# Optimization experiments

Measured on AMD Instinct MI355X. Metric: run time of the kernel, lower is better.

## Reference

```python
import jax, jax.numpy as jnp
import numpy as np

NUM_EXPERTS = 8
EMBED_DIM = 1024
EXPERT_DIM = 2048
TOP_K = 2
B, T = 2, 1024


def setup_inputs() -> dict:
    key = jax.random.key(0)
    ks = jax.random.split(key, 7)
    std = 0.02
    return {
        "x": jax.random.normal(ks[0], (B, T, EMBED_DIM), dtype=jnp.float32),
        "gate_inputs": jax.random.normal(ks[1], (B, T, EMBED_DIM), dtype=jnp.float32),
        "gate_kernel": jax.random.normal(ks[2], (EMBED_DIM, NUM_EXPERTS), dtype=jnp.float32) * std,
        "per_expert_scale": jnp.ones((NUM_EXPERTS,), dtype=jnp.float32),
        "gate_proj_w": jax.random.normal(ks[3], (NUM_EXPERTS, EMBED_DIM, EXPERT_DIM), dtype=jnp.float32) * std,
        "up_proj_w": jax.random.normal(ks[4], (NUM_EXPERTS, EMBED_DIM, EXPERT_DIM), dtype=jnp.float32) * std,
        "down_proj_w": jax.random.normal(ks[5], (NUM_EXPERTS, EXPERT_DIM, EMBED_DIM), dtype=jnp.float32) * std,
    }


def reference(x, gate_inputs, gate_kernel, per_expert_scale,
              gate_proj_w, up_proj_w, down_proj_w):
    Bb, Tt, D = x.shape
    x_flat = x.reshape(Bb * Tt, D)          # [t, e]
    g_flat = gate_inputs.reshape(Bb * Tt, D)

    logits = jnp.dot(g_flat, gate_kernel)   # [t, n]
    topk_logits, topk_idx = jax.lax.top_k(logits, TOP_K)  # [t, k]
    weights = jax.nn.sigmoid(topk_logits)   # [t, k]

    # Dense all-expert projections (as in the original module)
    gate_out = jnp.einsum('te,ned->tnd', x_flat, gate_proj_w)  # [t, n, d]
    up_out = jnp.einsum('te,ned->tnd', x_flat, up_proj_w)
    act = jax.nn.gelu(gate_out) * up_out
    expert_out = jnp.einsum('tnd,nde->tne', act, down_proj_w)  # [t, n, e]
    expert_out = expert_out * per_expert_scale[None, :, None]

    mask = jax.nn.one_hot(topk_idx, NUM_EXPERTS, dtype=expert_out.dtype)  # [t, k, n]
    selected = jnp.einsum('tkn,tne->tke', mask, expert_out)               # [t, k, e]
    out = jnp.einsum('tk,tke->te', weights, selected)                     # [t, e]
    return out.reshape(Bb, Tt, D)
```

## Files before the change

### kernel.cpp

```cpp
#include <hip/hip_runtime.h>
#include <math.h>
#include <stdint.h>

#define NE 8
#define ED 1024
#define FD 2048
#define NTOK 2048
#define BM 128
#define BN 128
#define BK 64

typedef unsigned short u16;
typedef unsigned int u32;
typedef __attribute__((ext_vector_type(4))) float f32x4;
typedef __attribute__((ext_vector_type(8))) short s16x8;
typedef __attribute__((ext_vector_type(4))) unsigned int u32v4;


__device__ __forceinline__ u16 f2bf(float f) {
    u32 u = __builtin_bit_cast(u32, f);
    u32 r = u + 0x7fffu + ((u >> 16) & 1u);
    return (u16)(r >> 16);
}

typedef __attribute__((address_space(1))) const void gvoid_t;
typedef __attribute__((address_space(3))) void lvoid_t;

__device__ __forceinline__ void gload16(const void* g, void* l) {
    __builtin_amdgcn_global_load_lds((gvoid_t*)g, (lvoid_t*)l, 16, 0, 0);
}


#define WS_CNT 0u
#define WS_OFF 64u
#define WS_TOK 256u
#define WS_WT  65792u
#define WS_XB  131328u
#define WS_WG  (8u << 20)
#define WS_WU  41943040u
#define WS_WD  75497472u
#define WS_ACT 109051904u
#define WS_NEED 130023424u


__global__ __launch_bounds__(256) void k_router(
        const float* __restrict__ gin, const float* __restrict__ gk,
        int* __restrict__ cnt, int* __restrict__ tok, float* __restrict__ wl) {
    int lane = threadIdx.x & 63;
    int t = (blockIdx.x * 256 + threadIdx.x) >> 6;
    if (t >= NTOK) return;
    const float* row = gin + (size_t)t * ED;
    float acc[NE];
#pragma unroll
    for (int e = 0; e < NE; e++) acc[e] = 0.f;
    for (int i = lane; i < ED; i += 64) {
        float v = row[i];
        const float* g = gk + i * NE;
#pragma unroll
        for (int e = 0; e < NE; e++) acc[e] = fmaf(v, g[e], acc[e]);
    }
#pragma unroll
    for (int e = 0; e < NE; e++) {
#pragma unroll
        for (int off = 32; off > 0; off >>= 1)
            acc[e] += __shfl_down(acc[e], off, 64);
    }
    if (lane == 0) {
        int b0 = 0; float v0 = acc[0];
#pragma unroll
        for (int e = 1; e < NE; e++) if (acc[e] > v0) { v0 = acc[e]; b0 = e; }
        int b1 = -1; float v1 = -3.4e38f;
#pragma unroll
        for (int e = 0; e < NE; e++) if (e != b0 && acc[e] > v1) { v1 = acc[e]; b1 = e; }
        float w0 = 1.f / (1.f + __expf(-v0));
        float w1 = 1.f / (1.f + __expf(-v1));
        int p0 = atomicAdd(&cnt[b0], 1);
        tok[b0 * NTOK + p0] = t; wl[b0 * NTOK + p0] = w0;
        int p1 = atomicAdd(&cnt[b1], 1);
        tok[b1 * NTOK + p1] = t; wl[b1 * NTOK + p1] = w1;
    }
}

__global__ void k_scan(const int* __restrict__ cnt, int* __restrict__ off) {
    if (threadIdx.x == 0 && blockIdx.x == 0) {
        int a = 0;
#pragma unroll
        for (int e = 0; e < NE; e++) { off[e] = a; a += (cnt[e] + 127) & ~127; }
        off[NE] = a;
    }
}


__global__ __launch_bounds__(256) void k_cvtx(const float4* __restrict__ x, uint2* __restrict__ xb) {
    int i = blockIdx.x * 256 + threadIdx.x;
    float4 v = x[i];
    uint2 o;
    o.x = (u32)f2bf(v.x) | ((u32)f2bf(v.y) << 16);
    o.y = (u32)f2bf(v.z) | ((u32)f2bf(v.w) << 16);
    xb[i] = o;
}


__global__ __launch_bounds__(256) void k_cvtw(
        const float* __restrict__ wgf, const float* __restrict__ wuf, const float* __restrict__ wdf,
        u16* __restrict__ og, u16* __restrict__ ou, u16* __restrict__ od) {
    int b = blockIdx.x;
    const float* src; u16* dst; int NT, KC, ROW;
    if (b < 2048)      { src = wgf; dst = og; NT = 16; KC = 16; ROW = FD; }
    else if (b < 4096) { b -= 2048; src = wuf; dst = ou; NT = 16; KC = 16; ROW = FD; }
    else               { b -= 4096; src = wdf; dst = od; NT = 8;  KC = 32; ROW = ED; }
    int ib = b;
    int kc = b % KC; int r = b / KC; int nt = r % NT; int e = r / NT;
    const float* base = src + (size_t)e * (size_t)(KC * 64) * ROW + (size_t)kc * 64 * ROW + nt * 128;
    u16* ob = dst + (size_t)ib * 8192;

    int tid = threadIdx.x;
    int p = tid & 7;
    int nsub = (tid >> 3) & 7;
    int w = tid >> 6;
    int k0 = (p ^ nsub) * 8;
    const float* rp = base + (size_t)k0 * ROW;

#pragma unroll
    for (int jg = 0; jg < 4; jg++) {
        int n = jg * 32 + w * 8 + nsub;
        float v[8];
#pragma unroll
        for (int i = 0; i < 8; i++) v[i] = rp[(size_t)i * ROW + n];
        u32 wd[4];
#pragma unroll
        for (int j = 0; j < 4; j++)
            wd[j] = (u32)f2bf(v[2 * j]) | ((u32)f2bf(v[2 * j + 1]) << 16);
        *(u32v4*)(ob + (size_t)n * 64 + p * 8) = (u32v4){wd[0], wd[1], wd[2], wd[3]};
    }
}


__global__ __launch_bounds__(256, 2) void k_passA(
        const u16* __restrict__ xb, const u16* __restrict__ wg, const u16* __restrict__ wu,
        const int* __restrict__ cnt, const int* __restrict__ off,
        const int* __restrict__ tok, u16* __restrict__ act) {
    int e = blockIdx.z, mt = blockIdx.y, nt = blockIdx.x;
    int c = cnt[e];
    if (mt * BM >= c) return;
    int rmax = c - mt * BM; if (rmax > BM) rmax = BM;

    __shared__ u16 sA[BM * BK];
    __shared__ u16 sBg[BN * BK];
    __shared__ u16 sBu[BN * BK];

    int tid = threadIdx.x;
    int lane = tid & 63, wv = tid >> 6;
    int wm = wv >> 1, wn = wv & 1;
    int col = lane & 15, quad = lane >> 4;
    int swz = col & 7;

    f32x4 zero = {0.f, 0.f, 0.f, 0.f};
    f32x4 ag[4][4], au[4][4];
#pragma unroll
    for (int i = 0; i < 4; i++)
#pragma unroll
        for (int j = 0; j < 4; j++) { ag[i][j] = zero; au[i][j] = zero; }

    int am = tid >> 1, ah = tid & 1;
    int ridx = mt * BM + am; if (ridx > c - 1) ridx = c - 1;
    int trow = tok[e * NTOK + ridx];
    const u16* asrc = xb + (size_t)trow * ED + ah * 32;
    u16* adst = sA + am * BK;

    const u16* gg = wg + ((size_t)(e * 16 + nt) * 16) * 8192;
    const u16* gu = wu + ((size_t)(e * 16 + nt) * 16) * 8192;
    const u16* bsrc0 = (wv < 2 ? gg : gu);
    int bhalf = (wv & 1) * 4096;
    u16* bdst = (wv < 2 ? sBg : sBu) + bhalf;

    for (int kc = 0; kc < 16; kc++) {
        __syncthreads();
        const u16* bs = bsrc0 + (size_t)kc * 8192 + bhalf + lane * 8;
#pragma unroll
        for (int i = 0; i < 8; i++)
            gload16(bs + i * 512, bdst + i * 512);
        const u16* as = asrc + kc * 64;
#pragma unroll
        for (int j = 0; j < 4; j++) {
            int pg = (ah * 4 + j) ^ (am & 7);
            *(u32v4*)(adst + pg * 8) = *(const u32v4*)(as + j * 8);
        }
        __syncthreads();
#pragma unroll
        for (int st = 0; st < 2; st++) {
            int poff = ((st * 4 + quad) ^ swz) * 8;
            s16x8 af[4];
#pragma unroll
            for (int mf = 0; mf < 4; mf++)
                af[mf] = *(const s16x8*)(sA + (wm * 64 + mf * 16 + col) * BK + poff);
#pragma unroll
            for (int nf = 0; nf < 4; nf++) {
                int brow = (wn * 64 + nf * 16 + col) * BK + poff;
                s16x8 bg = *(const s16x8*)(sBg + brow);
                s16x8 bu = *(const s16x8*)(sBu + brow);
#pragma unroll
                for (int mf = 0; mf < 4; mf++) {
                    ag[mf][nf] = __builtin_amdgcn_mfma_f32_16x16x32_bf16(af[mf], bg, ag[mf][nf], 0, 0, 0);
                    au[mf][nf] = __builtin_amdgcn_mfma_f32_16x16x32_bf16(af[mf], bu, au[mf][nf], 0, 0, 0);
                }
            }
        }
    }

    int tile = (off[e] >> 7) + mt;
    u16* ab = act + (size_t)tile * (32 * 8192);
#pragma unroll
    for (int mf = 0; mf < 4; mf++) {
#pragma unroll
        for (int reg = 0; reg < 4; reg++) {
            int m = wm * 64 + mf * 16 + quad * 4 + reg;
            if (m < rmax) {
#pragma unroll
                for (int nf = 0; nf < 4; nf++) {
                    float gv = ag[mf][nf][reg];
                    float uv = au[mf][nf][reg];
                    float z = 0.7978845608028654f * (gv + 0.044715f * gv * gv * gv);
                    float ez = __expf(-2.f * fabsf(z));
                    float th = (1.f - ez) / (1.f + ez);
                    th = (z < 0.f) ? -th : th;
                    float a = 0.5f * gv * (1.f + th) * uv;
                    int ng = nt * 128 + wn * 64 + nf * 16 + col;
                    int pos = ((((ng >> 3) & 7) ^ (m & 7)) * 8) | (ng & 7);
                    ab[(size_t)(ng >> 6) * 8192 + (size_t)m * 64 + pos] = f2bf(a);
                }
            }
        }
    }
}


__global__ __launch_bounds__(256, 3) void k_passB(
        const u16* __restrict__ act, const u16* __restrict__ wd,
        const int* __restrict__ cnt, const int* __restrict__ off,
        const int* __restrict__ tok, const float* __restrict__ wl,
        const float* __restrict__ scale, float* __restrict__ out) {
    int e = blockIdx.z, mt = blockIdx.y, nt = blockIdx.x;
    int c = cnt[e];
    if (mt * BM >= c) return;
    int rmax = c - mt * BM; if (rmax > BM) rmax = BM;

    __shared__ u16 sA[BM * BK];
    __shared__ u16 sB[BN * BK];

    int tid = threadIdx.x;
    int lane = tid & 63, wv = tid >> 6;
    int wm = wv >> 1, wn = wv & 1;
    int col = lane & 15, quad = lane >> 4;
    int swz = col & 7;

    f32x4 zero = {0.f, 0.f, 0.f, 0.f};
    f32x4 acc[4][4];
#pragma unroll
    for (int i = 0; i < 4; i++)
#pragma unroll
        for (int j = 0; j < 4; j++) acc[i][j] = zero;

    int tile = (off[e] >> 7) + mt;
    const u16* ga = act + (size_t)tile * (32 * 8192);
    const u16* gb = wd + ((size_t)(e * 8 + nt) * 32) * 8192;
    const u16* src0 = (wv < 2 ? ga : gb);
    int shalf = (wv & 1) * 4096;
    u16* dst0 = (wv < 2 ? sA : sB) + shalf;

    for (int kc = 0; kc < 32; kc++) {
        __syncthreads();
        const u16* s = src0 + (size_t)kc * 8192 + shalf + lane * 8;
#pragma unroll
        for (int i = 0; i < 8; i++)
            gload16(s + i * 512, dst0 + i * 512);
        __syncthreads();
#pragma unroll
        for (int st = 0; st < 2; st++) {
            int poff = ((st * 4 + quad) ^ swz) * 8;
            s16x8 af[4];
#pragma unroll
            for (int mf = 0; mf < 4; mf++)
                af[mf] = *(const s16x8*)(sA + (wm * 64 + mf * 16 + col) * BK + poff);
#pragma unroll
            for (int nf = 0; nf < 4; nf++) {
                int brow = (wn * 64 + nf * 16 + col) * BK + poff;
                s16x8 bf = *(const s16x8*)(sB + brow);
#pragma unroll
                for (int mf = 0; mf < 4; mf++)
                    acc[mf][nf] = __builtin_amdgcn_mfma_f32_16x16x32_bf16(af[mf], bf, acc[mf][nf], 0, 0, 0);
            }
        }
    }

    float sc = scale[e];
    int lbase = e * NTOK + mt * BM;
#pragma unroll
    for (int mf = 0; mf < 4; mf++) {
#pragma unroll
        for (int reg = 0; reg < 4; reg++) {
            int m = wm * 64 + mf * 16 + quad * 4 + reg;
            if (m < rmax) {
                int t = tok[lbase + m];
                float w = wl[lbase + m] * sc;
                float* orow = out + (size_t)t * ED + nt * 128 + wn * 64 + col;
#pragma unroll
                for (int nf = 0; nf < 4; nf++)
                    atomicAdd(orow + nf * 16, acc[mf][nf][reg] * w);
            }
        }
    }
}


extern "C" void kernel_launch(void* const* d_in, const int* in_sizes, int n_in,
                              void* d_out, int out_size, void* d_ws, size_t ws_size,
                              hipStream_t stream) {
    const float* x   = (const float*)d_in[0];
    const float* gin = (const float*)d_in[1];
    const float* gk  = (const float*)d_in[2];
    const float* sc  = (const float*)d_in[3];
    const float* wgf = (const float*)d_in[4];
    const float* wuf = (const float*)d_in[5];
    const float* wdf = (const float*)d_in[6];
    float* out = (float*)d_out;

    if (ws_size < (size_t)WS_NEED) {
        hipMemsetAsync(d_out, 0, (size_t)out_size * sizeof(float), stream);
        return;
    }

    char* ws = (char*)d_ws;
    int*   cnt = (int*)(ws + WS_CNT);
    int*   off = (int*)(ws + WS_OFF);
    int*   tok = (int*)(ws + WS_TOK);
    float* wl  = (float*)(ws + WS_WT);
    u16*   xb  = (u16*)(ws + WS_XB);
    u16*   og  = (u16*)(ws + WS_WG);
    u16*   ou  = (u16*)(ws + WS_WU);
    u16*   od  = (u16*)(ws + WS_WD);
    u16*   act = (u16*)(ws + WS_ACT);

    hipMemsetAsync(cnt, 0, 64, stream);
    hipMemsetAsync(d_out, 0, (size_t)out_size * sizeof(float), stream);

    k_cvtw<<<dim3(6144), dim3(256), 0, stream>>>(wgf, wuf, wdf, og, ou, od);
    k_router<<<dim3(512), dim3(256), 0, stream>>>(gin, gk, cnt, tok, wl);
    k_scan<<<dim3(1), dim3(64), 0, stream>>>(cnt, off);
    k_cvtx<<<dim3(2048), dim3(256), 0, stream>>>((const float4*)x, (uint2*)xb);
    k_passA<<<dim3(16, 16, NE), dim3(256), 0, stream>>>(xb, og, ou, cnt, off, tok, act);
    k_passB<<<dim3(8, 16, NE), dim3(256), 0, stream>>>(act, od, cnt, off, tok, wl, sc, out);
}
```

Baseline: 421.9 us.

## Shrink MoE GEMM N-tiles, split-K down proj, LDS-transpose weight conversion

```diff
diff --git a/kernel.cpp b/kernel.cpp
--- a/kernel.cpp
+++ b/kernel.cpp
@@ -7,7 +7,6 @@
 #define FD 2048
 #define NTOK 2048
 #define BM 128
-#define BN 128
 #define BK 64
 
 typedef unsigned short u16;
@@ -114,19 +113,32 @@
     const float* base = src + (size_t)e * (size_t)(KC * 64) * ROW + (size_t)kc * 64 * ROW + nt * 128;
     u16* ob = dst + (size_t)ib * 8192;
 
+    __shared__ float sl[64 * 128];
     int tid = threadIdx.x;
-    int p = tid & 7;
-    int nsub = (tid >> 3) & 7;
-    int w = tid >> 6;
-    int k0 = (p ^ nsub) * 8;
-    const float* rp = base + (size_t)k0 * ROW;
+
+    {
+        int rb = tid >> 5;
+        int c  = tid & 31;
+        const float* rp = base + (size_t)(8 * rb) * ROW + c * 4;
+        float* lp = sl + (8 * rb) * 128 + ((c ^ rb) << 2);
+#pragma unroll
+        for (int j = 0; j < 8; j++) {
+            float4 v = *(const float4*)(rp + (size_t)j * ROW);
+            *(float4*)(lp + j * 128) = v;
+        }
+    }
+    __syncthreads();
 
 #pragma unroll
     for (int jg = 0; jg < 4; jg++) {
-        int n = jg * 32 + w * 8 + nsub;
+        int o = jg * 256 + tid;
+        int n = o >> 3, p = o & 7;
+        int g = p ^ (n & 7);
+        int w = ((((n >> 2) ^ g) << 2) | (n & 3));
+        const float* kp = sl + (8 * g) * 128 + w;
         float v[8];
 #pragma unroll
-        for (int i = 0; i < 8; i++) v[i] = rp[(size_t)i * ROW + n];
+        for (int j = 0; j < 8; j++) v[j] = kp[j * 128];
         u32 wd[4];
 #pragma unroll
         for (int j = 0; j < 4; j++)
@@ -136,18 +148,19 @@
 }
 
 
-__global__ __launch_bounds__(256, 2) void k_passA(
+__global__ __launch_bounds__(256, 3) void k_passA(
         const u16* __restrict__ xb, const u16* __restrict__ wg, const u16* __restrict__ wu,
         const int* __restrict__ cnt, const int* __restrict__ off,
         const int* __restrict__ tok, u16* __restrict__ act) {
-    int e = blockIdx.z, mt = blockIdx.y, nt = blockIdx.x;
+    int flat = blockIdx.x;
+    int mt = flat >> 8; int rr = flat & 255; int e = rr >> 5; int nt = rr & 31;
     int c = cnt[e];
     if (mt * BM >= c) return;
     int rmax = c - mt * BM; if (rmax > BM) rmax = BM;
 
     __shared__ u16 sA[BM * BK];
-    __shared__ u16 sBg[BN * BK];
-    __shared__ u16 sBu[BN * BK];
+    __shared__ u16 sBg[64 * BK];
+    __shared__ u16 sBu[64 * BK];
 
     int tid = threadIdx.x;
     int lane = tid & 63, wv = tid >> 6;
@@ -156,11 +169,11 @@
     int swz = col & 7;
 
     f32x4 zero = {0.f, 0.f, 0.f, 0.f};
-    f32x4 ag[4][4], au[4][4];
+    f32x4 ag[4][2], au[4][2];
 #pragma unroll
     for (int i = 0; i < 4; i++)
 #pragma unroll
-        for (int j = 0; j < 4; j++) { ag[i][j] = zero; au[i][j] = zero; }
+        for (int j = 0; j < 2; j++) { ag[i][j] = zero; au[i][j] = zero; }
 
     int am = tid >> 1, ah = tid & 1;
     int ridx = mt * BM + am; if (ridx > c - 1) ridx = c - 1;
@@ -168,17 +181,17 @@
     const u16* asrc = xb + (size_t)trow * ED + ah * 32;
     u16* adst = sA + am * BK;
 
-    const u16* gg = wg + ((size_t)(e * 16 + nt) * 16) * 8192;
-    const u16* gu = wu + ((size_t)(e * 16 + nt) * 16) * 8192;
+    const u16* gg = wg + ((size_t)(e * 16 + (nt >> 1)) * 16) * 8192 + (nt & 1) * 4096;
+    const u16* gu = wu + ((size_t)(e * 16 + (nt >> 1)) * 16) * 8192 + (nt & 1) * 4096;
     const u16* bsrc0 = (wv < 2 ? gg : gu);
-    int bhalf = (wv & 1) * 4096;
+    int bhalf = (wv & 1) * 2048;
     u16* bdst = (wv < 2 ? sBg : sBu) + bhalf;
 
     for (int kc = 0; kc < 16; kc++) {
         __syncthreads();
         const u16* bs = bsrc0 + (size_t)kc * 8192 + bhalf + lane * 8;
 #pragma unroll
-        for (int i = 0; i < 8; i++)
+        for (int i = 0; i < 4; i++)
             gload16(bs + i * 512, bdst + i * 512);
         const u16* as = asrc + kc * 64;
 #pragma unroll
@@ -195,8 +208,8 @@
             for (int mf = 0; mf < 4; mf++)
                 af[mf] = *(const s16x8*)(sA + (wm * 64 + mf * 16 + col) * BK + poff);
 #pragma unroll
-            for (int nf = 0; nf < 4; nf++) {
-                int brow = (wn * 64 + nf * 16 + col) * BK + poff;
+            for (int nf = 0; nf < 2; nf++) {
+                int brow = (wn * 32 + nf * 16 + col) * BK + poff;
                 s16x8 bg = *(const s16x8*)(sBg + brow);
                 s16x8 bu = *(const s16x8*)(sBu + brow);
 #pragma unroll
@@ -217,7 +230,7 @@
             int m = wm * 64 + mf * 16 + quad * 4 + reg;
             if (m < rmax) {
 #pragma unroll
-                for (int nf = 0; nf < 4; nf++) {
+                for (int nf = 0; nf < 2; nf++) {
                     float gv = ag[mf][nf][reg];
                     float uv = au[mf][nf][reg];
                     float z = 0.7978845608028654f * (gv + 0.044715f * gv * gv * gv);
@@ -225,9 +238,9 @@
                     float th = (1.f - ez) / (1.f + ez);
                     th = (z < 0.f) ? -th : th;
                     float a = 0.5f * gv * (1.f + th) * uv;
-                    int ng = nt * 128 + wn * 64 + nf * 16 + col;
+                    int ng = nt * 64 + wn * 32 + nf * 16 + col;
                     int pos = ((((ng >> 3) & 7) ^ (m & 7)) * 8) | (ng & 7);
-                    ab[(size_t)(ng >> 6) * 8192 + (size_t)m * 64 + pos] = f2bf(a);
+                    ab[(size_t)nt * 8192 + (size_t)m * 64 + pos] = f2bf(a);
                 }
             }
         }
@@ -235,18 +248,20 @@
 }
 
 
-__global__ __launch_bounds__(256, 3) void k_passB(
+__global__ __launch_bounds__(256, 4) void k_passB(
         const u16* __restrict__ act, const u16* __restrict__ wd,
         const int* __restrict__ cnt, const int* __restrict__ off,
         const int* __restrict__ tok, const float* __restrict__ wl,
         const float* __restrict__ scale, float* __restrict__ out) {
-    int e = blockIdx.z, mt = blockIdx.y, nt = blockIdx.x;
+    int flat = blockIdx.x;
+    int g2 = flat >> 7; int nt = g2 >> 1; int kh = g2 & 1;
+    int rr = flat & 127; int e = rr >> 4; int mt = rr & 15;
     int c = cnt[e];
     if (mt * BM >= c) return;
     int rmax = c - mt * BM; if (rmax > BM) rmax = BM;
 
     __shared__ u16 sA[BM * BK];
-    __shared__ u16 sB[BN * BK];
+    __shared__ u16 sB[64 * BK];
 
     int tid = threadIdx.x;
     int lane = tid & 63, wv = tid >> 6;
@@ -255,25 +270,28 @@
     int swz = col & 7;
 
     f32x4 zero = {0.f, 0.f, 0.f, 0.f};
-    f32x4 acc[4][4];
+    f32x4 acc[4][2];
 #pragma unroll
     for (int i = 0; i < 4; i++)
 #pragma unroll
-        for (int j = 0; j < 4; j++) acc[i][j] = zero;
+        for (int j = 0; j < 2; j++) acc[i][j] = zero;
 
     int tile = (off[e] >> 7) + mt;
-    const u16* ga = act + (size_t)tile * (32 * 8192);
-    const u16* gb = wd + ((size_t)(e * 8 + nt) * 32) * 8192;
-    const u16* src0 = (wv < 2 ? ga : gb);
-    int shalf = (wv & 1) * 4096;
-    u16* dst0 = (wv < 2 ? sA : sB) + shalf;
-
-    for (int kc = 0; kc < 32; kc++) {
+    const u16* ga = act + (size_t)tile * (32 * 8192) + wv * 2048;
+    const u16* gb = wd + ((size_t)(e * 8 + (nt >> 1)) * 32) * 8192 + (nt & 1) * 4096 + wv * 1024;
+    u16* da = sA + wv * 2048;
+    u16* db = sB + wv * 1024;
+
+    for (int kc = kh * 16; kc < kh * 16 + 16; kc++) {
         __syncthreads();
-        const u16* s = src0 + (size_t)kc * 8192 + shalf + lane * 8;
-#pragma unroll
-        for (int i = 0; i < 8; i++)
-            gload16(s + i * 512, dst0 + i * 512);
+        const u16* a = ga + (size_t)kc * 8192 + lane * 8;
+#pragma unroll
+        for (int i = 0; i < 4; i++)
+            gload16(a + i * 512, da + i * 512);
+        const u16* bsrc = gb + (size_t)kc * 8192 + lane * 8;
+#pragma unroll
+        for (int i = 0; i < 2; i++)
+            gload16(bsrc + i * 512, db + i * 512);
         __syncthreads();
 #pragma unroll
         for (int st = 0; st < 2; st++) {
@@ -283,8 +301,8 @@
             for (int mf = 0; mf < 4; mf++)
                 af[mf] = *(const s16x8*)(sA + (wm * 64 + mf * 16 + col) * BK + poff);
 #pragma unroll
-            for (int nf = 0; nf < 4; nf++) {
-                int brow = (wn * 64 + nf * 16 + col) * BK + poff;
+            for (int nf = 0; nf < 2; nf++) {
+                int brow = (wn * 32 + nf * 16 + col) * BK + poff;
                 s16x8 bf = *(const s16x8*)(sB + brow);
 #pragma unroll
                 for (int mf = 0; mf < 4; mf++)
@@ -303,9 +321,9 @@
             if (m < rmax) {
                 int t = tok[lbase + m];
                 float w = wl[lbase + m] * sc;
-                float* orow = out + (size_t)t * ED + nt * 128 + wn * 64 + col;
-#pragma unroll
-                for (int nf = 0; nf < 4; nf++)
+                float* orow = out + (size_t)t * ED + nt * 64 + wn * 32 + col;
+#pragma unroll
+                for (int nf = 0; nf < 2; nf++)
                     atomicAdd(orow + nf * 16, acc[mf][nf][reg] * w);
             }
         }
@@ -344,10 +362,10 @@
     hipMemsetAsync(cnt, 0, 64, stream);
     hipMemsetAsync(d_out, 0, (size_t)out_size * sizeof(float), stream);
 
-    k_cvtw<<<dim3(6144), dim3(256), 0, stream>>>(wgf, wuf, wdf, og, ou, od);
     k_router<<<dim3(512), dim3(256), 0, stream>>>(gin, gk, cnt, tok, wl);
     k_scan<<<dim3(1), dim3(64), 0, stream>>>(cnt, off);
     k_cvtx<<<dim3(2048), dim3(256), 0, stream>>>((const float4*)x, (uint2*)xb);
-    k_passA<<<dim3(16, 16, NE), dim3(256), 0, stream>>>(xb, og, ou, cnt, off, tok, act);
-    k_passB<<<dim3(8, 16, NE), dim3(256), 0, stream>>>(act, od, cnt, off, tok, wl, sc, out);
-}
+    k_cvtw<<<dim3(6144), dim3(256), 0, stream>>>(wgf, wuf, wdf, og, ou, od);
+    k_passA<<<dim3(4096), dim3(256), 0, stream>>>(xb, og, ou, cnt, off, tok, act);
+    k_passB<<<dim3(4096), dim3(256), 0, stream>>>(act, od, cnt, off, tok, wl, sc, out);
+}
```

Result: slower. 454.5 us (+7.7%).

## Drop weight pre-conversion pass; read fp32 weights directly in MoE GEMMs

Applied to the files above, without the earlier changes.

```diff
diff --git a/kernel.cpp b/kernel.cpp
--- a/kernel.cpp
+++ b/kernel.cpp
@@ -6,9 +6,6 @@
 #define ED 1024
 #define FD 2048
 #define NTOK 2048
-#define BM 128
-#define BN 128
-#define BK 64
 
 typedef unsigned short u16;
 typedef unsigned int u32;
@@ -23,24 +20,21 @@
     return (u16)(r >> 16);
 }
 
-typedef __attribute__((address_space(1))) const void gvoid_t;
-typedef __attribute__((address_space(3))) void lvoid_t;
-
-__device__ __forceinline__ void gload16(const void* g, void* l) {
-    __builtin_amdgcn_global_load_lds((gvoid_t*)g, (lvoid_t*)l, 16, 0, 0);
-}
-
+__device__ __forceinline__ s16x8 pack8(const float* v) {
+    union { s16x8 s; u32 w[4]; } u;
+#pragma unroll
+    for (int i = 0; i < 4; i++)
+        u.w[i] = (u32)f2bf(v[2 * i]) | ((u32)f2bf(v[2 * i + 1]) << 16);
+    return u.s;
+}
 
 #define WS_CNT 0u
 #define WS_OFF 64u
 #define WS_TOK 256u
 #define WS_WT  65792u
 #define WS_XB  131328u
-#define WS_WG  (8u << 20)
-#define WS_WU  41943040u
-#define WS_WD  75497472u
-#define WS_ACT 109051904u
-#define WS_NEED 130023424u
+#define WS_ACT 4325632u
+#define WS_NEED 21102848u
 
 
 __global__ __launch_bounds__(256) void k_router(
@@ -85,7 +79,7 @@
     if (threadIdx.x == 0 && blockIdx.x == 0) {
         int a = 0;
 #pragma unroll
-        for (int e = 0; e < NE; e++) { off[e] = a; a += (cnt[e] + 127) & ~127; }
+        for (int e = 0; e < NE; e++) { off[e] = a; a += (cnt[e] + 255) & ~255; }
         off[NE] = a;
     }
 }
@@ -101,53 +95,17 @@
 }
 
 
-__global__ __launch_bounds__(256) void k_cvtw(
-        const float* __restrict__ wgf, const float* __restrict__ wuf, const float* __restrict__ wdf,
-        u16* __restrict__ og, u16* __restrict__ ou, u16* __restrict__ od) {
-    int b = blockIdx.x;
-    const float* src; u16* dst; int NT, KC, ROW;
-    if (b < 2048)      { src = wgf; dst = og; NT = 16; KC = 16; ROW = FD; }
-    else if (b < 4096) { b -= 2048; src = wuf; dst = ou; NT = 16; KC = 16; ROW = FD; }
-    else               { b -= 4096; src = wdf; dst = od; NT = 8;  KC = 32; ROW = ED; }
-    int ib = b;
-    int kc = b % KC; int r = b / KC; int nt = r % NT; int e = r / NT;
-    const float* base = src + (size_t)e * (size_t)(KC * 64) * ROW + (size_t)kc * 64 * ROW + nt * 128;
-    u16* ob = dst + (size_t)ib * 8192;
-
-    int tid = threadIdx.x;
-    int p = tid & 7;
-    int nsub = (tid >> 3) & 7;
-    int w = tid >> 6;
-    int k0 = (p ^ nsub) * 8;
-    const float* rp = base + (size_t)k0 * ROW;
-
-#pragma unroll
-    for (int jg = 0; jg < 4; jg++) {
-        int n = jg * 32 + w * 8 + nsub;
-        float v[8];
-#pragma unroll
-        for (int i = 0; i < 8; i++) v[i] = rp[(size_t)i * ROW + n];
-        u32 wd[4];
-#pragma unroll
-        for (int j = 0; j < 4; j++)
-            wd[j] = (u32)f2bf(v[2 * j]) | ((u32)f2bf(v[2 * j + 1]) << 16);
-        *(u32v4*)(ob + (size_t)n * 64 + p * 8) = (u32v4){wd[0], wd[1], wd[2], wd[3]};
-    }
-}
-
-
 __global__ __launch_bounds__(256, 2) void k_passA(
-        const u16* __restrict__ xb, const u16* __restrict__ wg, const u16* __restrict__ wu,
+        const u16* __restrict__ xb, const float* __restrict__ wgf, const float* __restrict__ wuf,
         const int* __restrict__ cnt, const int* __restrict__ off,
         const int* __restrict__ tok, u16* __restrict__ act) {
-    int e = blockIdx.z, mt = blockIdx.y, nt = blockIdx.x;
+    int flat = blockIdx.x;
+    int nt = flat & 31; int r = flat >> 5; int e = r & 7; int mt = r >> 3;
     int c = cnt[e];
-    if (mt * BM >= c) return;
-    int rmax = c - mt * BM; if (rmax > BM) rmax = BM;
-
-    __shared__ u16 sA[BM * BK];
-    __shared__ u16 sBg[BN * BK];
-    __shared__ u16 sBu[BN * BK];
+    if (mt * 256 >= c) return;
+    int rmax = c - mt * 256; if (rmax > 256) rmax = 256;
+
+    __shared__ u16 sA[256 * 64];
 
     int tid = threadIdx.x;
     int lane = tid & 63, wv = tid >> 6;
@@ -156,68 +114,72 @@
     int swz = col & 7;
 
     f32x4 zero = {0.f, 0.f, 0.f, 0.f};
-    f32x4 ag[4][4], au[4][4];
-#pragma unroll
-    for (int i = 0; i < 4; i++)
-#pragma unroll
-        for (int j = 0; j < 4; j++) { ag[i][j] = zero; au[i][j] = zero; }
-
-    int am = tid >> 1, ah = tid & 1;
-    int ridx = mt * BM + am; if (ridx > c - 1) ridx = c - 1;
+    f32x4 ag[8][2], au[8][2];
+#pragma unroll
+    for (int i = 0; i < 8; i++)
+#pragma unroll
+        for (int j = 0; j < 2; j++) { ag[i][j] = zero; au[i][j] = zero; }
+
+    int ridx = mt * 256 + tid; if (ridx > c - 1) ridx = c - 1;
     int trow = tok[e * NTOK + ridx];
-    const u16* asrc = xb + (size_t)trow * ED + ah * 32;
-    u16* adst = sA + am * BK;
-
-    const u16* gg = wg + ((size_t)(e * 16 + nt) * 16) * 8192;
-    const u16* gu = wu + ((size_t)(e * 16 + nt) * 16) * 8192;
-    const u16* bsrc0 = (wv < 2 ? gg : gu);
-    int bhalf = (wv & 1) * 4096;
-    u16* bdst = (wv < 2 ? sBg : sBu) + bhalf;
+    const u16* asrc = xb + (size_t)trow * ED;
+    u16* adst = sA + tid * 64;
+    int am7 = tid & 7;
+
+    const float* wgB = wgf + (size_t)e * (ED * FD) + nt * 64 + wn * 32 + col;
+    const float* wuB = wuf + (size_t)e * (ED * FD) + nt * 64 + wn * 32 + col;
 
     for (int kc = 0; kc < 16; kc++) {
+        const u16* as = asrc + kc * 64;
+        u32v4 pa[8];
+#pragma unroll
+        for (int j = 0; j < 8; j++) pa[j] = *(const u32v4*)(as + j * 8);
         __syncthreads();
-        const u16* bs = bsrc0 + (size_t)kc * 8192 + bhalf + lane * 8;
-#pragma unroll
-        for (int i = 0; i < 8; i++)
-            gload16(bs + i * 512, bdst + i * 512);
-        const u16* as = asrc + kc * 64;
-#pragma unroll
-        for (int j = 0; j < 4; j++) {
-            int pg = (ah * 4 + j) ^ (am & 7);
-            *(u32v4*)(adst + pg * 8) = *(const u32v4*)(as + j * 8);
-        }
+#pragma unroll
+        for (int j = 0; j < 8; j++)
+            *(u32v4*)(adst + ((j ^ am7) << 3)) = pa[j];
         __syncthreads();
 #pragma unroll
         for (int st = 0; st < 2; st++) {
             int poff = ((st * 4 + quad) ^ swz) * 8;
-            s16x8 af[4];
-#pragma unroll
-            for (int mf = 0; mf < 4; mf++)
-                af[mf] = *(const s16x8*)(sA + (wm * 64 + mf * 16 + col) * BK + poff);
-#pragma unroll
-            for (int nf = 0; nf < 4; nf++) {
-                int brow = (wn * 64 + nf * 16 + col) * BK + poff;
-                s16x8 bg = *(const s16x8*)(sBg + brow);
-                s16x8 bu = *(const s16x8*)(sBu + brow);
-#pragma unroll
-                for (int mf = 0; mf < 4; mf++) {
-                    ag[mf][nf] = __builtin_amdgcn_mfma_f32_16x16x32_bf16(af[mf], bg, ag[mf][nf], 0, 0, 0);
-                    au[mf][nf] = __builtin_amdgcn_mfma_f32_16x16x32_bf16(af[mf], bu, au[mf][nf], 0, 0, 0);
-                }
+            s16x8 af[8];
+#pragma unroll
+            for (int mf = 0; mf < 8; mf++)
+                af[mf] = *(const s16x8*)(sA + (wm * 128 + mf * 16 + col) * 64 + poff);
+            size_t kbase = (size_t)(kc * 64 + st * 32 + quad * 8);
+#pragma unroll
+            for (int nf = 0; nf < 2; nf++) {
+                float bv[8];
+#pragma unroll
+                for (int j = 0; j < 8; j++) bv[j] = wgB[(kbase + j) * FD + nf * 16];
+                s16x8 bf = pack8(bv);
+#pragma unroll
+                for (int mf = 0; mf < 8; mf++)
+                    ag[mf][nf] = __builtin_amdgcn_mfma_f32_16x16x32_bf16(af[mf], bf, ag[mf][nf], 0, 0, 0);
+            }
+#pragma unroll
+            for (int nf = 0; nf < 2; nf++) {
+                float bv[8];
+#pragma unroll
+                for (int j = 0; j < 8; j++) bv[j] = wuB[(kbase + j) * FD + nf * 16];
+                s16x8 bf = pack8(bv);
+#pragma unroll
+                for (int mf = 0; mf < 8; mf++)
+                    au[mf][nf] = __builtin_amdgcn_mfma_f32_16x16x32_bf16(af[mf], bf, au[mf][nf], 0, 0, 0);
             }
         }
     }
 
-    int tile = (off[e] >> 7) + mt;
-    u16* ab = act + (size_t)tile * (32 * 8192);
-#pragma unroll
-    for (int mf = 0; mf < 4; mf++) {
+    int rbase = off[e] + mt * 256;
+#pragma unroll
+    for (int mf = 0; mf < 8; mf++) {
 #pragma unroll
         for (int reg = 0; reg < 4; reg++) {
-            int m = wm * 64 + mf * 16 + quad * 4 + reg;
+            int m = wm * 128 + mf * 16 + quad * 4 + reg;
             if (m < rmax) {
-#pragma unroll
-                for (int nf = 0; nf < 4; nf++) {
+                u16* arow = act + (size_t)(rbase + m) * FD + nt * 64 + wn * 32 + col;
+#pragma unroll
+                for (int nf = 0; nf < 2; nf++) {
                     float gv = ag[mf][nf][reg];
                     float uv = au[mf][nf][reg];
                     float z = 0.7978845608028654f * (gv + 0.044715f * gv * gv * gv);
@@ -225,9 +187,7 @@
                     float th = (1.f - ez) / (1.f + ez);
                     th = (z < 0.f) ? -th : th;
                     float a = 0.5f * gv * (1.f + th) * uv;
-                    int ng = nt * 128 + wn * 64 + nf * 16 + col;
-                    int pos = ((((ng >> 3) & 7) ^ (m & 7)) * 8) | (ng & 7);
-                    ab[(size_t)(ng >> 6) * 8192 + (size_t)m * 64 + pos] = f2bf(a);
+                    arow[nf * 16] = f2bf(a);
                 }
             }
         }
@@ -236,17 +196,17 @@
 
 
 __global__ __launch_bounds__(256, 3) void k_passB(
-        const u16* __restrict__ act, const u16* __restrict__ wd,
+        const u16* __restrict__ act, const float* __restrict__ wdf,
         const int* __restrict__ cnt, const int* __restrict__ off,
         const int* __restrict__ tok, const float* __restrict__ wl,
         const float* __restrict__ scale, float* __restrict__ out) {
-    int e = blockIdx.z, mt = blockIdx.y, nt = blockIdx.x;
+    int flat = blockIdx.x;
+    int nt = flat & 15; int r = flat >> 4; int e = r & 7; int mt = r >> 3;
     int c = cnt[e];
-    if (mt * BM >= c) return;
-    int rmax = c - mt * BM; if (rmax > BM) rmax = BM;
-
-    __shared__ u16 sA[BM * BK];
-    __shared__ u16 sB[BN * BK];
+    if (mt * 128 >= c) return;
+    int rmax = c - mt * 128; if (rmax > 128) rmax = 128;
+
+    __shared__ u16 sA[128 * 64];
 
     int tid = threadIdx.x;
     int lane = tid & 63, wv = tid >> 6;
@@ -255,25 +215,28 @@
     int swz = col & 7;
 
     f32x4 zero = {0.f, 0.f, 0.f, 0.f};
-    f32x4 acc[4][4];
+    f32x4 acc[4][2];
 #pragma unroll
     for (int i = 0; i < 4; i++)
 #pragma unroll
-        for (int j = 0; j < 4; j++) acc[i][j] = zero;
-
-    int tile = (off[e] >> 7) + mt;
-    const u16* ga = act + (size_t)tile * (32 * 8192);
-    const u16* gb = wd + ((size_t)(e * 8 + nt) * 32) * 8192;
-    const u16* src0 = (wv < 2 ? ga : gb);
-    int shalf = (wv & 1) * 4096;
-    u16* dst0 = (wv < 2 ? sA : sB) + shalf;
+        for (int j = 0; j < 2; j++) acc[i][j] = zero;
+
+    int am = tid >> 1, ah = tid & 1;
+    const u16* asrc = act + (size_t)(off[e] + mt * 128 + am) * FD + ah * 32;
+    u16* adst = sA + am * 64;
+    int am7 = am & 7;
+
+    const float* wdB = wdf + (size_t)e * (FD * ED) + nt * 64 + wn * 32 + col;
 
     for (int kc = 0; kc < 32; kc++) {
+        const u16* as = asrc + kc * 64;
+        u32v4 pa[4];
+#pragma unroll
+        for (int j = 0; j < 4; j++) pa[j] = *(const u32v4*)(as + j * 8);
         __syncthreads();
-        const u16* s = src0 + (size_t)kc * 8192 + shalf + lane * 8;
-#pragma unroll
-        for (int i = 0; i < 8; i++)
-            gload16(s + i * 512, dst0 + i * 512);
+#pragma unroll
+        for (int j = 0; j < 4; j++)
+            *(u32v4*)(adst + (((ah * 4 + j) ^ am7) << 3)) = pa[j];
         __syncthreads();
 #pragma unroll
         for (int st = 0; st < 2; st++) {
@@ -281,11 +244,14 @@
             s16x8 af[4];
 #pragma unroll
             for (int mf = 0; mf < 4; mf++)
-                af[mf] = *(const s16x8*)(sA + (wm * 64 + mf * 16 + col) * BK + poff);
-#pragma unroll
-            for (int nf = 0; nf < 4; nf++) {
-                int brow = (wn * 64 + nf * 16 + col) * BK + poff;
-                s16x8 bf = *(const s16x8*)(sB + brow);
+                af[mf] = *(const s16x8*)(sA + (wm * 64 + mf * 16 + col) * 64 + poff);
+            size_t kbase = (size_t)(kc * 64 + st * 32 + quad * 8);
+#pragma unroll
+            for (int nf = 0; nf < 2; nf++) {
+                float bv[8];
+#pragma unroll
+                for (int j = 0; j < 8; j++) bv[j] = wdB[(kbase + j) * ED + nf * 16];
+                s16x8 bf = pack8(bv);
 #pragma unroll
                 for (int mf = 0; mf < 4; mf++)
                     acc[mf][nf] = __builtin_amdgcn_mfma_f32_16x16x32_bf16(af[mf], bf, acc[mf][nf], 0, 0, 0);
@@ -294,7 +260,7 @@
     }
 
     float sc = scale[e];
-    int lbase = e * NTOK + mt * BM;
+    int lbase = e * NTOK + mt * 128;
 #pragma unroll
     for (int mf = 0; mf < 4; mf++) {
 #pragma unroll
@@ -303,9 +269,9 @@
             if (m < rmax) {
                 int t = tok[lbase + m];
                 float w = wl[lbase + m] * sc;
-                float* orow = out + (size_t)t * ED + nt * 128 + wn * 64 + col;
-#pragma unroll
-                for (int nf = 0; nf < 4; nf++)
+                float* orow = out + (size_t)t * ED + nt * 64 + wn * 32 + col;
+#pragma unroll
+                for (int nf = 0; nf < 2; nf++)
                     atomicAdd(orow + nf * 16, acc[mf][nf][reg] * w);
             }
         }
@@ -336,18 +302,14 @@
     int*   tok = (int*)(ws + WS_TOK);
     float* wl  = (float*)(ws + WS_WT);
     u16*   xb  = (u16*)(ws + WS_XB);
-    u16*   og  = (u16*)(ws + WS_WG);
-    u16*   ou  = (u16*)(ws + WS_WU);
-    u16*   od  = (u16*)(ws + WS_WD);
     u16*   act = (u16*)(ws + WS_ACT);
 
     hipMemsetAsync(cnt, 0, 64, stream);
     hipMemsetAsync(d_out, 0, (size_t)out_size * sizeof(float), stream);
 
-    k_cvtw<<<dim3(6144), dim3(256), 0, stream>>>(wgf, wuf, wdf, og, ou, od);
     k_router<<<dim3(512), dim3(256), 0, stream>>>(gin, gk, cnt, tok, wl);
     k_scan<<<dim3(1), dim3(64), 0, stream>>>(cnt, off);
     k_cvtx<<<dim3(2048), dim3(256), 0, stream>>>((const float4*)x, (uint2*)xb);
-    k_passA<<<dim3(16, 16, NE), dim3(256), 0, stream>>>(xb, og, ou, cnt, off, tok, act);
-    k_passB<<<dim3(8, 16, NE), dim3(256), 0, stream>>>(act, od, cnt, off, tok, wl, sc, out);
-}
+    k_passA<<<dim3(2048), dim3(256), 0, stream>>>(xb, wgf, wuf, cnt, off, tok, act);
+    k_passB<<<dim3(2048), dim3(256), 0, stream>>>(act, wdf, cnt, off, tok, wl, sc, out);
+}
```

After: 486.0 us. +15.2%, slower.
